# Kernel optimization log

Measured on AMD Instinct MI355X. Metric: run time of the kernel, lower is better.

## Reference

```python
import jax, jax.numpy as jnp
import numpy as np

H, W, P, Q, K_STEP = 32, 32, 12, 12, 12
NUM_CELLS = H * W
TE_DEPTH = 24 * 7  # 168
# 8 neighbor directions: positions 0..8 of a 3x3 stencil, excluding center (4)
DIRS = [(r, c) for r in range(3) for c in range(3) if not (r == 1 and c == 1)]


def setup_inputs() -> dict:
    key = jax.random.key(0)
    k1, k2, k3, k4, k5, k6 = jax.random.split(key, 6)
    B = 4
    X = jax.random.uniform(k1, (B, P, H, W, 1), dtype=jnp.float32)
    day = jax.random.randint(k2, (B, P + Q, 1), 0, 7, dtype=jnp.int32)
    hour = jax.random.randint(k3, (B, P + Q, 1), 0, 24, dtype=jnp.int32)
    TE = jnp.concatenate([day, hour], axis=-1)  # [B, P+Q, 2]
    F = TE_DEPTH + NUM_CELLS  # 1192
    s = 1.0 / np.sqrt(F)
    W_trans = jax.random.normal(k4, (F, 8), dtype=jnp.float32) * s
    W_restart = jax.random.normal(k5, (F, 1), dtype=jnp.float32) * s
    W_bias = jax.random.normal(k6, (F, 1), dtype=jnp.float32) * s
    return {"X": X, "TE": TE, "W_trans": W_trans, "W_restart": W_restart, "W_bias": W_bias}


def _te_pos_P(TE, B, dtype):
    # one-hot time encoding [B,T,168] tiled over the grid
    te_idx = TE[..., 0] * 24 + TE[..., 1]
    te_oh = jax.nn.one_hot(te_idx, TE_DEPTH, dtype=dtype)  # [B,T,168]
    te_b = jnp.broadcast_to(te_oh[:, :P, None, None, :], (B, P, H, W, TE_DEPTH))
    # positional one-hot per cell: identity reshaped to [H,W,H*W]
    pos = jnp.eye(NUM_CELLS, dtype=dtype).reshape(H, W, NUM_CELLS)
    pos_b = jnp.broadcast_to(pos[None, None], (B, P, H, W, NUM_CELLS))
    return jnp.concatenate([te_b, pos_b], axis=-1)  # [B,P,H,W,1192]


def reference(X, TE, W_trans, W_restart, W_bias):
    B = X.shape[0]
    TE_pos_P = _te_pos_P(TE, B, X.dtype)
    trans_prob = jax.nn.softmax(TE_pos_P @ W_trans, axis=-1)      # [B,P,H,W,8]
    restart_prob = jax.nn.sigmoid(TE_pos_P @ W_restart)           # [B,P,H,W,1]
    X_bias = (TE_pos_P @ W_bias) * X                              # [B,P,H,W,1]
    x = X
    results = [x]
    for _ in range(K_STEP):
        xn = x * trans_prob                                       # [B,P,H,W,8]
        xn_pad = jnp.pad(xn, ((0, 0), (0, 0), (1, 1), (1, 1), (0, 0)))
        # 8-neighbor shift-gather (equivalent to the one-hot conv3d)
        x_trans = sum(xn_pad[:, :, r:r + H, c:c + W, d] for d, (r, c) in enumerate(DIRS))
        x_trans = x_trans[..., None]                              # [B,P,H,W,1]
        x = (1.0 - restart_prob) * x_trans + restart_prob * x + X_bias
        results.append(x)
    Y = x[:, -1:]
    return (Y, x, trans_prob[..., None], restart_prob, jnp.stack(results, axis=-1))
```

## Files before the change

### kernel.cpp

```cpp
#include <hip/hip_runtime.h>


namespace {
constexpr int PP  = 12;
constexpr int NC  = 1024;
constexpr int TED = 168;
constexpr int KS  = 12;
constexpr int PAD = 34;
constexpr long O_X   = 4096;
constexpr long O_TP  = 53248;
constexpr long O_RP  = 446464;
constexpr long O_RES = 495616;
}

__global__ __launch_bounds__(1024) void rwr_fused(
    const float* __restrict__ X,
    const int* __restrict__ TE,
    const float* __restrict__ Wt,
    const float* __restrict__ Wr,
    const float* __restrict__ Wb,
    float* __restrict__ out)
{
    __shared__ float tp[NC * 8];
    __shared__ float xb0[PAD * PAD];
    __shared__ float xb1[PAD * PAD];

    const int bp   = blockIdx.x;
    const int b    = bp / PP;
    const int p    = bp - b * PP;
    const int cell = threadIdx.x;
    const int h    = cell >> 5;
    const int w    = cell & 31;

    for (int i = threadIdx.x; i < PAD * PAD; i += 1024) { xb0[i] = 0.f; xb1[i] = 0.f; }
    __syncthreads();

    const int te = TE[(b * 24 + p) * 2 + 0] * 24 + TE[(b * 24 + p) * 2 + 1];

    float pr[8];
    float m = -1e30f;
    #pragma unroll
    for (int j = 0; j < 8; ++j) {
        pr[j] = Wt[te * 8 + j] + Wt[(TED + cell) * 8 + j];
        m = fmaxf(m, pr[j]);
    }
    float s = 0.f;
    #pragma unroll
    for (int j = 0; j < 8; ++j) { pr[j] = __expf(pr[j] - m); s += pr[j]; }
    const float inv = 1.f / s;
    #pragma unroll
    for (int j = 0; j < 8; ++j) { pr[j] *= inv; tp[cell * 8 + j] = pr[j]; }

    const float rp    = 1.f / (1.f + __expf(-(Wr[te] + Wr[TED + cell])));
    const float x0    = X[bp * NC + cell];
    const float xbias = (Wb[te] + Wb[TED + cell]) * x0;

    xb0[(h + 1) * PAD + (w + 1)] = x0;
    __syncthreads();

    const int drr[8] = {-1,-1,-1, 0, 0, 1, 1, 1};
    const int dcc[8] = {-1, 0, 1,-1, 1,-1, 0, 1};
    float wn[8];
    #pragma unroll
    for (int d = 0; d < 8; ++d) {
        const int nh = h + drr[d], nw = w + dcc[d];
        const bool ok = ((unsigned)nh < 32u) && ((unsigned)nw < 32u);
        const int nidx = ok ? (nh * 32 + nw) : 0;
        wn[d] = tp[nidx * 8 + d];
    }

    float res[KS + 1];
    res[0] = x0;
    float x = x0;
    float* cur = xb0;
    float* nxt = xb1;
    #pragma unroll
    for (int k = 0; k < KS; ++k) {
        float xt = 0.f;
        #pragma unroll
        for (int d = 0; d < 8; ++d)
            xt += wn[d] * cur[(h + 1 + drr[d]) * PAD + (w + 1 + dcc[d])];
        x = (1.f - rp) * xt + rp * x + xbias;
        res[k + 1] = x;
        nxt[(h + 1) * PAD + (w + 1)] = x;
        float* t = cur; cur = nxt; nxt = t;
        __syncthreads();
    }

    const long gci = (long)bp * NC + cell;
    out[O_X + gci] = x;
    #pragma unroll
    for (int j = 0; j < 8; ++j) out[O_TP + gci * 8 + j] = pr[j];
    out[O_RP + gci] = rp;
    #pragma unroll
    for (int k = 0; k <= KS; ++k) out[O_RES + gci * 13 + k] = res[k];
    if (p == PP - 1) out[(long)b * NC + cell] = x;
}

extern "C" void kernel_launch(void* const* d_in, const int* in_sizes, int n_in,
                              void* d_out, int out_size, void* d_ws, size_t ws_size,
                              hipStream_t stream) {
    const float* X  = (const float*)d_in[0];
    const int*   TE = (const int*)d_in[1];
    const float* Wt = (const float*)d_in[2];
    const float* Wr = (const float*)d_in[3];
    const float* Wb = (const float*)d_in[4];
    float* out = (float*)d_out;

    rwr_fused<<<dim3(4 * PP), dim3(1024), 0, stream>>>(X, TE, Wt, Wr, Wb, out);
}
```

Before: 68.95 us.

## Use 256-thread blocks with four cells per thread and interleaved output stores

Shrinks each block from 1024 to 256 threads, with every thread handling four cells spaced eight rows apart, so each of the 12 per-step barriers synchronises fewer waves. Only the halo border of the padded shared buffers is zeroed instead of the whole buffer. The transition-probability, restart and per-step result stores are issued inside the compute loop, overlapping global writes with the recurrence. This costs less thread-level parallelism per block, and only 48 blocks run, so more serial work falls on each thread.

```diff
diff --git a/kernel.cpp b/kernel.cpp
--- a/kernel.cpp
+++ b/kernel.cpp
@@ -13,7 +13,7 @@
 constexpr long O_RES = 495616;
 }
 
-__global__ __launch_bounds__(1024) void rwr_fused(
+__global__ __launch_bounds__(256) void rwr_fused(
     const float* __restrict__ X,
     const int* __restrict__ TE,
     const float* __restrict__ Wt,
@@ -25,76 +25,103 @@
     __shared__ float xb0[PAD * PAD];
     __shared__ float xb1[PAD * PAD];
 
-    const int bp   = blockIdx.x;
-    const int b    = bp / PP;
-    const int p    = bp - b * PP;
-    const int cell = threadIdx.x;
-    const int h    = cell >> 5;
-    const int w    = cell & 31;
+    const int bp = blockIdx.x;
+    const int b  = bp / PP;
+    const int p  = bp - b * PP;
+    const int t  = threadIdx.x;
+    const int w  = t & 31;
+    const int r0 = t >> 5;
 
-    for (int i = threadIdx.x; i < PAD * PAD; i += 1024) { xb0[i] = 0.f; xb1[i] = 0.f; }
-    __syncthreads();
+    if (t < 132) {
+        int idx;
+        if (t < 34)       idx = t;
+        else if (t < 68)  idx = 33 * PAD + (t - 34);
+        else { const int j = t - 68;
+               idx = ((j >> 1) + 1) * PAD + ((j & 1) ? 33 : 0); }
+        xb0[idx] = 0.f; xb1[idx] = 0.f;
+    }
 
     const int te = TE[(b * 24 + p) * 2 + 0] * 24 + TE[(b * 24 + p) * 2 + 1];
 
-    float pr[8];
-    float m = -1e30f;
+    float x[4], xbias[4], rp[4];
+    long  resbase[4];
+
     #pragma unroll
-    for (int j = 0; j < 8; ++j) {
-        pr[j] = Wt[te * 8 + j] + Wt[(TED + cell) * 8 + j];
-        m = fmaxf(m, pr[j]);
+    for (int i = 0; i < 4; ++i) {
+        const int  cell = t + 256 * i;
+        const int  h    = r0 + 8 * i;
+        const long gci  = (long)bp * NC + cell;
+
+        float pr[8]; float m = -1e30f;
+        #pragma unroll
+        for (int j = 0; j < 8; ++j) {
+            pr[j] = Wt[te * 8 + j] + Wt[(TED + cell) * 8 + j];
+            m = fmaxf(m, pr[j]);
+        }
+        float s = 0.f;
+        #pragma unroll
+        for (int j = 0; j < 8; ++j) { pr[j] = __expf(pr[j] - m); s += pr[j]; }
+        const float inv = 1.f / s;
+        #pragma unroll
+        for (int j = 0; j < 8; ++j) {
+            pr[j] *= inv;
+            tp[cell * 8 + j] = pr[j];
+            out[O_TP + gci * 8 + j] = pr[j];
+        }
+
+        rp[i] = 1.f / (1.f + __expf(-(Wr[te] + Wr[TED + cell])));
+        out[O_RP + gci] = rp[i];
+
+        const float x0 = X[bp * NC + cell];
+        x[i]     = x0;
+        xbias[i] = (Wb[te] + Wb[TED + cell]) * x0;
+        xb0[(h + 1) * PAD + (w + 1)] = x0;
+
+        resbase[i] = O_RES + gci * 13;
+        out[resbase[i]] = x0;
     }
-    float s = 0.f;
-    #pragma unroll
-    for (int j = 0; j < 8; ++j) { pr[j] = __expf(pr[j] - m); s += pr[j]; }
-    const float inv = 1.f / s;
-    #pragma unroll
-    for (int j = 0; j < 8; ++j) { pr[j] *= inv; tp[cell * 8 + j] = pr[j]; }
-
-    const float rp    = 1.f / (1.f + __expf(-(Wr[te] + Wr[TED + cell])));
-    const float x0    = X[bp * NC + cell];
-    const float xbias = (Wb[te] + Wb[TED + cell]) * x0;
-
-    xb0[(h + 1) * PAD + (w + 1)] = x0;
     __syncthreads();
 
     const int drr[8] = {-1,-1,-1, 0, 0, 1, 1, 1};
     const int dcc[8] = {-1, 0, 1,-1, 1,-1, 0, 1};
-    float wn[8];
+    float wn[4][8];
     #pragma unroll
-    for (int d = 0; d < 8; ++d) {
-        const int nh = h + drr[d], nw = w + dcc[d];
-        const bool ok = ((unsigned)nh < 32u) && ((unsigned)nw < 32u);
-        const int nidx = ok ? (nh * 32 + nw) : 0;
-        wn[d] = tp[nidx * 8 + d];
+    for (int i = 0; i < 4; ++i) {
+        const int h = r0 + 8 * i;
+        #pragma unroll
+        for (int d = 0; d < 8; ++d) {
+            const int nh = h + drr[d], nw = w + dcc[d];
+            const bool ok = ((unsigned)nh < 32u) && ((unsigned)nw < 32u);
+            const int nidx = ok ? (nh * 32 + nw) : 0;
+            wn[i][d] = tp[nidx * 8 + d];
+        }
     }
 
-    float res[KS + 1];
-    res[0] = x0;
-    float x = x0;
     float* cur = xb0;
     float* nxt = xb1;
     #pragma unroll
     for (int k = 0; k < KS; ++k) {
-        float xt = 0.f;
         #pragma unroll
-        for (int d = 0; d < 8; ++d)
-            xt += wn[d] * cur[(h + 1 + drr[d]) * PAD + (w + 1 + dcc[d])];
-        x = (1.f - rp) * xt + rp * x + xbias;
-        res[k + 1] = x;
-        nxt[(h + 1) * PAD + (w + 1)] = x;
-        float* t = cur; cur = nxt; nxt = t;
+        for (int i = 0; i < 4; ++i) {
+            const int base = (r0 + 8 * i + 1) * PAD + (w + 1);
+            float xt = 0.f;
+            #pragma unroll
+            for (int d = 0; d < 8; ++d)
+                xt += wn[i][d] * cur[base + drr[d] * PAD + dcc[d]];
+            x[i] = (1.f - rp[i]) * xt + rp[i] * x[i] + xbias[i];
+            nxt[base] = x[i];
+            out[resbase[i] + k + 1] = x[i];
+        }
+        float* tmp = cur; cur = nxt; nxt = tmp;
         __syncthreads();
     }
 
-    const long gci = (long)bp * NC + cell;
-    out[O_X + gci] = x;
     #pragma unroll
-    for (int j = 0; j < 8; ++j) out[O_TP + gci * 8 + j] = pr[j];
-    out[O_RP + gci] = rp;
-    #pragma unroll
-    for (int k = 0; k <= KS; ++k) out[O_RES + gci * 13 + k] = res[k];
-    if (p == PP - 1) out[(long)b * NC + cell] = x;
+    for (int i = 0; i < 4; ++i) {
+        const long gci = (long)bp * NC + t + 256 * i;
+        out[O_X + gci] = x[i];
+        if (p == PP - 1) out[(long)b * NC + t + 256 * i] = x[i];
+    }
 }
 
 extern "C" void kernel_launch(void* const* d_in, const int* in_sizes, int n_in,
@@ -107,5 +134,5 @@
     const float* Wb = (const float*)d_in[4];
     float* out = (float*)d_out;
 
-    rwr_fused<<<dim3(4 * PP), dim3(1024), 0, stream>>>(X, TE, Wt, Wr, Wb, out);
+    rwr_fused<<<dim3(4 * PP), dim3(256), 0, stream>>>(X, TE, Wt, Wr, Wb, out);
 }
```

Result: no change. 69.29 us (+0.5%).
